# Kernel optimization log

Hardware: AMD Instinct MI355X
Metric: run time of the kernel (lower is better)

Reference implementation:

```python
import jax, jax.numpy as jnp
import numpy as np

N, K, D = 262144, 1024, 64


def setup_inputs() -> dict:
    key = jax.random.key(0)
    k1, k2 = jax.random.split(key)
    input_data = jax.random.normal(k1, (N, D), dtype=jnp.float32)
    codewords = jax.random.normal(k2, (K, D), dtype=jnp.float32)
    return {"input_data": input_data, "codewords": codewords}


def reference(input_data, codewords):
    # input_data: [N, D], codewords: [K, D]
    x = input_data.reshape(-1, codewords.shape[1])
    x2 = jnp.sum(x * x, axis=1, keepdims=True)          # [N, 1]
    c2 = jnp.sum(codewords * codewords, axis=1)          # [K]
    d2 = x2 + c2[None, :] - 2.0 * (x @ codewords.T)      # [N, K]
    distances = jnp.sqrt(jnp.maximum(d2, 0.0))
    quantized_indices = jnp.argmin(distances, axis=1)    # [N] int
    quantized_distances = jnp.take_along_axis(
        distances, quantized_indices[:, None], axis=1
    )[:, 0]                                              # [N]
    quantized_data = codewords[quantized_indices]        # [N, D]
    return (quantized_indices, quantized_distances, quantized_data)
```

## Files before the change

### kernel.cpp

```cpp
#include <hip/hip_runtime.h>


#define N_PTS 262144
#define K_CW  1024
#define DIM   64
#define CHUNK_B 36864
#define C2_OFF  (8 * CHUNK_B)

typedef __attribute__((ext_vector_type(8)))  short short8;
typedef __attribute__((ext_vector_type(16))) float floatx16;

__device__ __forceinline__ unsigned short f2bf(float f) {
    unsigned u = __float_as_uint(f);
    return (unsigned short)((u + 0x7FFFu + ((u >> 16) & 1u)) >> 16);
}
__device__ __forceinline__ float bf2f(unsigned short h) {
    return __uint_as_float(((unsigned)h) << 16);
}
__device__ __forceinline__ float dot4(float4 a, float4 b) {
    return a.x*b.x + a.y*b.y + a.z*b.z + a.w*b.w;
}
__device__ __forceinline__ void async_cp16(const void* g, void* l) {
    __builtin_amdgcn_global_load_lds(
        (const __attribute__((address_space(1))) unsigned int*)g,
        (__attribute__((address_space(3))) unsigned int*)l, 16, 0, 0);
}

__global__ void vq_prep(const float* __restrict__ cw, unsigned char* __restrict__ ws) {
    const int k = blockIdx.x * 256 + threadIdx.x;
    const int ch = k >> 7, r = k & 127;
    unsigned short* chunk = (unsigned short*)(ws + (size_t)ch * CHUNK_B);
    unsigned short* hi = chunk + r * 72;
    unsigned short* lo = hi + 9216;
    const float4* cr = (const float4*)cw + (size_t)k * 16;
    float c2 = 0.f;
    #pragma unroll
    for (int j = 0; j < 16; ++j) {
        float4 v = cr[j];
        c2 += dot4(v, v);
        float4 m = make_float4(-2.f*v.x, -2.f*v.y, -2.f*v.z, -2.f*v.w);
        unsigned short h0 = f2bf(m.x), h1 = f2bf(m.y), h2 = f2bf(m.z), h3 = f2bf(m.w);
        unsigned short l0 = f2bf(m.x - bf2f(h0)), l1 = f2bf(m.y - bf2f(h1)),
                       l2 = f2bf(m.z - bf2f(h2)), l3 = f2bf(m.w - bf2f(h3));
        uint2 hv, lv;
        hv.x = (unsigned)h0 | ((unsigned)h1 << 16);
        hv.y = (unsigned)h2 | ((unsigned)h3 << 16);
        lv.x = (unsigned)l0 | ((unsigned)l1 << 16);
        lv.y = (unsigned)l2 | ((unsigned)l3 << 16);
        *(uint2*)(hi + j * 4) = hv;
        *(uint2*)(lo + j * 4) = lv;
    }
    ((float*)(ws + C2_OFF))[k] = c2;
}

__launch_bounds__(256, 2)
__global__ void vq_kernel(const float* __restrict__ x,
                          const float* __restrict__ cw,
                          const unsigned char* __restrict__ ws,
                          float* __restrict__ out) {
    __shared__ __align__(16) unsigned char sB[2 * CHUNK_B];
    int*   sci  = (int*)sB;
    float* sdd  = (float*)(sB + 2048);
    int*   sidx = (int*)(sB + 4096);

    const int tid  = threadIdx.x;
    const int w    = tid >> 6;
    const int lane = tid & 63;
    const int q    = lane >> 5;
    const int l31  = lane & 31;
    const int base = blockIdx.x * 256;
    const float4* __restrict__ x4  = (const float4*)x;
    const float4* __restrict__ c4p = (const float4*)cw;
    const float*  __restrict__ c2g = (const float*)(ws + C2_OFF);

    short8 ah[2][4], al[2][4];
    #pragma unroll
    for (int rt = 0; rt < 2; ++rt) {
        const int row = w * 64 + rt * 32 + l31;
        const float4* xr = x4 + (size_t)(base + row) * 16;
        #pragma unroll
        for (int ks = 0; ks < 4; ++ks) {
            float4 va = xr[ks * 4 + q * 2];
            float4 vb = xr[ks * 4 + q * 2 + 1];
            float f[8] = {va.x, va.y, va.z, va.w, vb.x, vb.y, vb.z, vb.w};
            short8 h, l;
            #pragma unroll
            for (int j = 0; j < 8; ++j) {
                unsigned short hb = f2bf(f[j]);
                h[j] = (short)hb;
                l[j] = (short)f2bf(f[j] - bf2f(hb));
            }
            ah[rt][ks] = h; al[rt][ks] = l;
        }
    }

    float bu[32];
    #pragma unroll
    for (int s = 0; s < 32; ++s) bu[s] = 3.4e38f;

    {
        const unsigned char* g = ws + w * 9216 + lane * 16;
        unsigned char* l = sB + w * 9216;
        #pragma unroll
        for (int i = 0; i < 9; ++i) async_cp16(g + i * 1024, l + i * 1024);
    }

    for (int ch = 0; ch < 8; ++ch) {
        __syncthreads();

        if (ch < 7) {
            const unsigned char* g = ws + (size_t)(ch + 1) * CHUNK_B + w * 9216 + lane * 16;
            unsigned char* l = sB + ((ch + 1) & 1) * CHUNK_B + w * 9216;
            #pragma unroll
            for (int i = 0; i < 9; ++i) async_cp16(g + i * 1024, l + i * 1024);
        }

        float c2v[4];
        #pragma unroll
        for (int ct = 0; ct < 4; ++ct) c2v[ct] = c2g[ch * 128 + ct * 32 + l31];

        const unsigned short* bufS = (const unsigned short*)(sB + (ch & 1) * CHUNK_B);

        #pragma unroll
        for (int ct = 0; ct < 4; ++ct) {
            const int nrow = ct * 32 + l31;
            short8 bh[4], bl[4];
            #pragma unroll
            for (int ks = 0; ks < 4; ++ks) {
                bh[ks] = *(const short8*)&bufS[nrow * 72 + ks * 16 + q * 8];
                bl[ks] = *(const short8*)&bufS[9216 + nrow * 72 + ks * 16 + q * 8];
            }
            floatx16 a0, a1;
            #pragma unroll
            for (int r = 0; r < 16; ++r) { a0[r] = c2v[ct]; a1[r] = c2v[ct]; }
            #pragma unroll
            for (int ks = 0; ks < 4; ++ks) {
                a0 = __builtin_amdgcn_mfma_f32_32x32x16_bf16(ah[0][ks], bh[ks], a0, 0, 0, 0);
                a1 = __builtin_amdgcn_mfma_f32_32x32x16_bf16(ah[1][ks], bh[ks], a1, 0, 0, 0);
                a0 = __builtin_amdgcn_mfma_f32_32x32x16_bf16(al[0][ks], bh[ks], a0, 0, 0, 0);
                a1 = __builtin_amdgcn_mfma_f32_32x32x16_bf16(al[1][ks], bh[ks], a1, 0, 0, 0);
                a0 = __builtin_amdgcn_mfma_f32_32x32x16_bf16(ah[0][ks], bl[ks], a0, 0, 0, 0);
                a1 = __builtin_amdgcn_mfma_f32_32x32x16_bf16(ah[1][ks], bl[ks], a1, 0, 0, 0);
            }
            const unsigned tch = (unsigned)(ch * 4 + ct);
            #pragma unroll
            for (int r = 0; r < 16; ++r) {
                unsigned u0 = (__float_as_uint(a0[r]) & 0xFFFFFFE0u) | tch;
                bu[r] = fminf(bu[r], __uint_as_float(u0));
                unsigned u1 = (__float_as_uint(a1[r]) & 0xFFFFFFE0u) | tch;
                bu[16 + r] = fminf(bu[16 + r], __uint_as_float(u1));
            }
        }
    }
    __syncthreads();

    #pragma unroll
    for (int s = 0; s < 32; ++s) {
        float b0 = bu[s];
        int i0 = (int)(((__float_as_uint(b0) & 31u) << 5) | (unsigned)l31);
        float b1 = 3.4e38f; int i1 = 0x7fffffff;
        #pragma unroll
        for (int m = 1; m < 32; m <<= 1) {
            float ob0 = __shfl_xor(b0, m); int oi0 = __shfl_xor(i0, m);
            float ob1 = __shfl_xor(b1, m); int oi1 = __shfl_xor(i1, m);
            bool t = (ob0 < b0) || (ob0 == b0 && oi0 < i0);
            float hs = t ? b0 : ob0; int hi_ = t ? i0 : oi0;
            b0 = t ? ob0 : b0;       i0 = t ? oi0 : i0;
            bool u = (ob1 < b1) || (ob1 == b1 && oi1 < i1);
            float ms = u ? ob1 : b1; int mi = u ? oi1 : i1;
            bool z = (hs < ms) || (hs == ms && hi_ < mi);
            b1 = z ? hs : ms; i1 = z ? hi_ : mi;
        }
        if (l31 == s) {
            const int rt = s >> 4, r = s & 15;
            const int row = w * 64 + rt * 32 + (r & 3) + 8 * (r >> 2) + 4 * q;
            sci[row * 2]     = i0;
            sci[row * 2 + 1] = i1;
        }
    }
    __syncthreads();

    #pragma unroll
    for (int it = 0; it < 2; ++it) {
        const int pid = it * 128 + (tid >> 1);
        const int h   = tid & 1;
        const int ia = sci[pid * 2], ib = sci[pid * 2 + 1];
        const float4* xr = x4 + (size_t)(base + pid) * 16 + h * 8;
        const float4* ca = c4p + (size_t)ia * 16 + h * 8;
        const float4* cb = c4p + (size_t)ib * 16 + h * 8;
        float da = 0.f, db = 0.f;
        #pragma unroll
        for (int j = 0; j < 8; ++j) {
            float4 xv = xr[j], av = ca[j], bv = cb[j];
            float4 d1 = make_float4(xv.x-av.x, xv.y-av.y, xv.z-av.z, xv.w-av.w);
            float4 d2 = make_float4(xv.x-bv.x, xv.y-bv.y, xv.z-bv.z, xv.w-bv.w);
            da += dot4(d1, d1);
            db += dot4(d2, d2);
        }
        da += __shfl_xor(da, 1);
        db += __shfl_xor(db, 1);
        if (h == 0) { sdd[pid * 2] = da; sdd[pid * 2 + 1] = db; }
    }
    __syncthreads();

    {
        const float da = sdd[tid * 2], db = sdd[tid * 2 + 1];
        const int   ia = sci[tid * 2], ib = sci[tid * 2 + 1];
        bool ta = (da < db) || (da == db && ia < ib);
        const int   bidx = ta ? ia : ib;
        const float bd   = ta ? da : db;
        out[base + tid]         = (float)bidx;
        out[N_PTS + base + tid] = sqrtf(fmaxf(bd, 0.f));
        sidx[tid] = bidx;
    }
    __syncthreads();

    {
        float4* od = (float4*)(out + 2 * (size_t)N_PTS) + (size_t)base * 16;
        #pragma unroll
        for (int i = 0; i < 16; ++i) {
            const int g = i * 256 + tid;
            od[g] = c4p[(size_t)sidx[g >> 4] * 16 + (g & 15)];
        }
    }
}

extern "C" void kernel_launch(void* const* d_in, const int* in_sizes, int n_in,
                              void* d_out, int out_size, void* d_ws, size_t ws_size,
                              hipStream_t stream) {
    const float* x  = (const float*)d_in[0];
    const float* cw = (const float*)d_in[1];
    float* out = (float*)d_out;
    unsigned char* ws = (unsigned char*)d_ws;
    vq_prep<<<4, 256, 0, stream>>>(cw, ws);
    vq_kernel<<<N_PTS / 256, 256, 0, stream>>>(x, cw, ws, out);
}
```

Before: 246.7 us.

## Stream codebook fragments straight into registers, replacing LDS double-buffering

Drops the async global-to-LDS double-buffered codebook staging and its per-chunk block barriers. The codebook image becomes one contiguous 256-byte row per codeword, and each lane loads its MFMA B fragments directly from global memory. A two-deep register buffer prefetches the next 32-codeword tile while the current one is computed. This removes LDS traffic and synchronisation, but all four waves now read the same codebook data through the caches, and the last prefetch reads past the codebook image into the c2 region and beyond.

```diff
diff --git a/kernel.cpp b/kernel.cpp
--- a/kernel.cpp
+++ b/kernel.cpp
@@ -4,8 +4,8 @@
 #define N_PTS 262144
 #define K_CW  1024
 #define DIM   64
-#define CHUNK_B 36864
-#define C2_OFF  (8 * CHUNK_B)
+#define IMG_ROW_B 256
+#define C2_OFF  (K_CW * IMG_ROW_B)
 
 typedef __attribute__((ext_vector_type(8)))  short short8;
 typedef __attribute__((ext_vector_type(16))) float floatx16;
@@ -20,18 +20,11 @@
 __device__ __forceinline__ float dot4(float4 a, float4 b) {
     return a.x*b.x + a.y*b.y + a.z*b.z + a.w*b.w;
 }
-__device__ __forceinline__ void async_cp16(const void* g, void* l) {
-    __builtin_amdgcn_global_load_lds(
-        (const __attribute__((address_space(1))) unsigned int*)g,
-        (__attribute__((address_space(3))) unsigned int*)l, 16, 0, 0);
-}
 
 __global__ void vq_prep(const float* __restrict__ cw, unsigned char* __restrict__ ws) {
     const int k = blockIdx.x * 256 + threadIdx.x;
-    const int ch = k >> 7, r = k & 127;
-    unsigned short* chunk = (unsigned short*)(ws + (size_t)ch * CHUNK_B);
-    unsigned short* hi = chunk + r * 72;
-    unsigned short* lo = hi + 9216;
+    unsigned short* hi = (unsigned short*)(ws + (size_t)k * IMG_ROW_B);
+    unsigned short* lo = hi + 64;
     const float4* cr = (const float4*)cw + (size_t)k * 16;
     float c2 = 0.f;
     #pragma unroll
@@ -53,15 +46,47 @@
     ((float*)(ws + C2_OFF))[k] = c2;
 }
 
+__device__ __forceinline__ void loadB(const unsigned char* __restrict__ p,
+                                      short8 h[4], short8 l[4]) {
+    #pragma unroll
+    for (int ks = 0; ks < 4; ++ks) {
+        h[ks] = *(const short8*)(p + ks * 32);
+        l[ks] = *(const short8*)(p + 128 + ks * 32);
+    }
+}
+
+__device__ __forceinline__ void compute_ct(const short8 ah[2][4], const short8 al[2][4],
+                                           const short8 Bh[4], const short8 Bl[4],
+                                           float c2v, unsigned tag, float bu[32]) {
+    floatx16 a0, a1;
+    #pragma unroll
+    for (int r = 0; r < 16; ++r) { a0[r] = c2v; a1[r] = c2v; }
+    #pragma unroll
+    for (int ks = 0; ks < 4; ++ks) {
+        a0 = __builtin_amdgcn_mfma_f32_32x32x16_bf16(ah[0][ks], Bh[ks], a0, 0, 0, 0);
+        a1 = __builtin_amdgcn_mfma_f32_32x32x16_bf16(ah[1][ks], Bh[ks], a1, 0, 0, 0);
+        a0 = __builtin_amdgcn_mfma_f32_32x32x16_bf16(al[0][ks], Bh[ks], a0, 0, 0, 0);
+        a1 = __builtin_amdgcn_mfma_f32_32x32x16_bf16(al[1][ks], Bh[ks], a1, 0, 0, 0);
+        a0 = __builtin_amdgcn_mfma_f32_32x32x16_bf16(ah[0][ks], Bl[ks], a0, 0, 0, 0);
+        a1 = __builtin_amdgcn_mfma_f32_32x32x16_bf16(ah[1][ks], Bl[ks], a1, 0, 0, 0);
+    }
+    #pragma unroll
+    for (int r = 0; r < 16; ++r) {
+        unsigned u0 = (__float_as_uint(a0[r]) & 0xFFFFFFE0u) | tag;
+        bu[r] = fminf(bu[r], __uint_as_float(u0));
+        unsigned u1 = (__float_as_uint(a1[r]) & 0xFFFFFFE0u) | tag;
+        bu[16 + r] = fminf(bu[16 + r], __uint_as_float(u1));
+    }
+}
+
 __launch_bounds__(256, 2)
 __global__ void vq_kernel(const float* __restrict__ x,
                           const float* __restrict__ cw,
                           const unsigned char* __restrict__ ws,
                           float* __restrict__ out) {
-    __shared__ __align__(16) unsigned char sB[2 * CHUNK_B];
-    int*   sci  = (int*)sB;
-    float* sdd  = (float*)(sB + 2048);
-    int*   sidx = (int*)(sB + 4096);
+    __shared__ int   sci[512];
+    __shared__ float sdd[512];
+    __shared__ int   sidx[256];
 
     const int tid  = threadIdx.x;
     const int w    = tid >> 6;
@@ -71,7 +96,6 @@
     const int base = blockIdx.x * 256;
     const float4* __restrict__ x4  = (const float4*)x;
     const float4* __restrict__ c4p = (const float4*)cw;
-    const float*  __restrict__ c2g = (const float*)(ws + C2_OFF);
 
     short8 ah[2][4], al[2][4];
     #pragma unroll
@@ -98,61 +122,24 @@
     #pragma unroll
     for (int s = 0; s < 32; ++s) bu[s] = 3.4e38f;
 
-    {
-        const unsigned char* g = ws + w * 9216 + lane * 16;
-        unsigned char* l = sB + w * 9216;
-        #pragma unroll
-        for (int i = 0; i < 9; ++i) async_cp16(g + i * 1024, l + i * 1024);
-    }
-
-    for (int ch = 0; ch < 8; ++ch) {
-        __syncthreads();
-
-        if (ch < 7) {
-            const unsigned char* g = ws + (size_t)(ch + 1) * CHUNK_B + w * 9216 + lane * 16;
-            unsigned char* l = sB + ((ch + 1) & 1) * CHUNK_B + w * 9216;
-            #pragma unroll
-            for (int i = 0; i < 9; ++i) async_cp16(g + i * 1024, l + i * 1024);
-        }
-
-        float c2v[4];
-        #pragma unroll
-        for (int ct = 0; ct < 4; ++ct) c2v[ct] = c2g[ch * 128 + ct * 32 + l31];
-
-        const unsigned short* bufS = (const unsigned short*)(sB + (ch & 1) * CHUNK_B);
-
-        #pragma unroll
-        for (int ct = 0; ct < 4; ++ct) {
-            const int nrow = ct * 32 + l31;
-            short8 bh[4], bl[4];
-            #pragma unroll
-            for (int ks = 0; ks < 4; ++ks) {
-                bh[ks] = *(const short8*)&bufS[nrow * 72 + ks * 16 + q * 8];
-                bl[ks] = *(const short8*)&bufS[9216 + nrow * 72 + ks * 16 + q * 8];
-            }
-            floatx16 a0, a1;
-            #pragma unroll
-            for (int r = 0; r < 16; ++r) { a0[r] = c2v[ct]; a1[r] = c2v[ct]; }
-            #pragma unroll
-            for (int ks = 0; ks < 4; ++ks) {
-                a0 = __builtin_amdgcn_mfma_f32_32x32x16_bf16(ah[0][ks], bh[ks], a0, 0, 0, 0);
-                a1 = __builtin_amdgcn_mfma_f32_32x32x16_bf16(ah[1][ks], bh[ks], a1, 0, 0, 0);
-                a0 = __builtin_amdgcn_mfma_f32_32x32x16_bf16(al[0][ks], bh[ks], a0, 0, 0, 0);
-                a1 = __builtin_amdgcn_mfma_f32_32x32x16_bf16(al[1][ks], bh[ks], a1, 0, 0, 0);
-                a0 = __builtin_amdgcn_mfma_f32_32x32x16_bf16(ah[0][ks], bl[ks], a0, 0, 0, 0);
-                a1 = __builtin_amdgcn_mfma_f32_32x32x16_bf16(ah[1][ks], bl[ks], a1, 0, 0, 0);
-            }
-            const unsigned tch = (unsigned)(ch * 4 + ct);
-            #pragma unroll
-            for (int r = 0; r < 16; ++r) {
-                unsigned u0 = (__float_as_uint(a0[r]) & 0xFFFFFFE0u) | tch;
-                bu[r] = fminf(bu[r], __uint_as_float(u0));
-                unsigned u1 = (__float_as_uint(a1[r]) & 0xFFFFFFE0u) | tch;
-                bu[16 + r] = fminf(bu[16 + r], __uint_as_float(u1));
-            }
-        }
-    }
-    __syncthreads();
+    const unsigned char* bp = ws + (size_t)l31 * IMG_ROW_B + q * 16;
+    const float* c2p = (const float*)(ws + C2_OFF) + l31;
+
+    short8 B0h[4], B0l[4], B1h[4], B1l[4];
+    float c2a, c2b;
+    loadB(bp, B0h, B0l);
+    c2a = c2p[0];
+
+    #pragma unroll 1
+    for (int ct = 0; ct < 32; ct += 2) {
+        loadB(bp + 8192, B1h, B1l);
+        c2b = c2p[(ct + 1) * 32];
+        compute_ct(ah, al, B0h, B0l, c2a, (unsigned)ct, bu);
+        loadB(bp + 16384, B0h, B0l);
+        c2a = c2p[(ct + 2) * 32];
+        compute_ct(ah, al, B1h, B1l, c2b, (unsigned)(ct + 1), bu);
+        bp += 16384;
+    }
 
     #pragma unroll
     for (int s = 0; s < 32; ++s) {
```

After: 300.5 us. 1.22x slower.
